# Optimization experiments

Measured on AMD Instinct MI355X. Metric: run time of the kernel, lower is better.

## Reference

```python
import jax, jax.numpy as jnp
import numpy as np

B, S, D, H = 2, 2048, 1024, 16
HD = D // H
SCALE = float(np.sqrt(HD))


def setup_inputs() -> dict:
    key = jax.random.key(0)
    k_x, k_wqkv, k_bqkv, k_wo, k_bo = jax.random.split(key, 5)
    std = 1.0 / np.sqrt(D)
    x = jax.random.normal(k_x, (B, S, D), dtype=jnp.float32)
    mask = jnp.tril(jnp.ones((S, S), dtype=jnp.int32))[None, None]  # (1,1,S,S) causal
    W_qkv = jax.random.normal(k_wqkv, (D, 3 * D), dtype=jnp.float32) * std
    b_qkv = jax.random.normal(k_bqkv, (3 * D,), dtype=jnp.float32) * std
    W_o = jax.random.normal(k_wo, (D, D), dtype=jnp.float32) * std
    b_o = jax.random.normal(k_bo, (D,), dtype=jnp.float32) * std
    return {"x": x, "W_qkv": W_qkv, "b_qkv": b_qkv, "W_o": W_o, "b_o": b_o, "mask": mask}


def reference(x, W_qkv, b_qkv, W_o, b_o, mask):
    # fused QKV projection: (B,S,3D) -> (3,B,H,S,HD)
    qkv = x @ W_qkv + b_qkv
    qkv = qkv.reshape(B, S, 3, H, HD).transpose(2, 0, 3, 1, 4)
    Q, K, V = qkv[0], qkv[1], qkv[2]
    # scaled dot-product attention with explicit mask
    scores = jnp.einsum('bhqd,bhkd->bhqk', Q, K) / SCALE
    scores = jnp.where(mask == 0, -jnp.inf, scores)
    attn = jax.nn.softmax(scores, axis=-1)  # dropout p=0.0 -> identity
    context = jnp.einsum('bhqk,bhkd->bhqd', attn, V)
    context = context.transpose(0, 2, 1, 3).reshape(B, S, D)
    return context @ W_o + b_o
```

## Files before the change

### kernel.cpp

```cpp
#include <hip/hip_runtime.h>
#include <hip/hip_bf16.h>
#include <stdint.h>

#define DEV __device__ __forceinline__

typedef __bf16 bf16x8 __attribute__((ext_vector_type(8)));
typedef float f32x4 __attribute__((ext_vector_type(4)));
typedef float f32x16 __attribute__((ext_vector_type(16)));
typedef unsigned short ushort8 __attribute__((ext_vector_type(8)));

DEV uint16_t f2bf(float f) {
  uint32_t u = __float_as_uint(f);
  u += 0x7fffu + ((u >> 16) & 1u);
  return (uint16_t)(u >> 16);
}

DEV float exp2r(float x) {
  float r;
  asm("v_exp_f32 %0, %1" : "=v"(r) : "v"(x));
  return r;
}

DEV void gload_lds16(const void* g, void* l) {
  __builtin_amdgcn_global_load_lds(
      (const __attribute__((address_space(1))) void*)g,
      (__attribute__((address_space(3))) void*)l, 16, 0, 0);
}

DEV void swap32u(uint32_t& a, uint32_t& b) {
#if defined(__has_builtin) && __has_builtin(__builtin_amdgcn_permlane32_swap)
  auto r = __builtin_amdgcn_permlane32_swap(a, b, false, false);
  a = (uint32_t)r[0];
  b = (uint32_t)r[1];
#else
  uint32_t as = __shfl_xor(a, 32), bs = __shfl_xor(b, 32);
  uint32_t na = (threadIdx.x & 32) ? bs : a;
  uint32_t nb = (threadIdx.x & 32) ? b : as;
  a = na; b = nb;
#endif
}

__global__ __launch_bounds__(256) void k_prep(const float* __restrict__ W0,
                                              uint16_t* __restrict__ WT0,
                                              const float* __restrict__ W1,
                                              uint16_t* __restrict__ WT1,
                                              const float* __restrict__ X,
                                              uint16_t* __restrict__ Xb) {
  const int z = blockIdx.z;
  const int tid = threadIdx.x;
  if (z == 2) {
    const int nt4 = 1048576, stride = 48 * 16 * 256;
    int base = (blockIdx.y * 48 + blockIdx.x) * 256 + tid;
    for (int i = base; i < nt4; i += stride) {
      float4 v = *reinterpret_cast<const float4*>(X + (size_t)i * 4);
      ushort4 o = { f2bf(v.x), f2bf(v.y), f2bf(v.z), f2bf(v.w) };
      *reinterpret_cast<ushort4*>(Xb + (size_t)i * 4) = o;
    }
    return;
  }
  if (z == 1 && blockIdx.x >= 16) return;
  const float* W = z ? W1 : W0;
  uint16_t* WT = z ? WT1 : WT0;
  const int K = 1024, N = z ? 1024 : 3072;
  __shared__ float t[64][65];
  int n0 = blockIdx.x * 64, k0 = blockIdx.y * 64;
  int r = tid >> 4, c4 = (tid & 15) * 4;
#pragma unroll
  for (int p = 0; p < 4; ++p) {
    int kr = p * 16 + r;
    float4 v = *reinterpret_cast<const float4*>(W + (size_t)(k0 + kr) * N + n0 + c4);
    t[kr][c4] = v.x; t[kr][c4 + 1] = v.y; t[kr][c4 + 2] = v.z; t[kr][c4 + 3] = v.w;
  }
  __syncthreads();
#pragma unroll
  for (int p = 0; p < 4; ++p) {
    int nr = p * 16 + r;
    ushort4 o = { f2bf(t[c4][nr]), f2bf(t[c4 + 1][nr]), f2bf(t[c4 + 2][nr]), f2bf(t[c4 + 3][nr]) };
    *reinterpret_cast<ushort4*>(WT + (size_t)(n0 + nr) * K + k0 + c4) = o;
  }
}

__global__ __launch_bounds__(256, 2) void k_gemm0(const uint16_t* __restrict__ A,
                                                  const uint16_t* __restrict__ Bw,
                                                  const float* __restrict__ bias,
                                                  uint16_t* __restrict__ o0,
                                                  uint16_t* __restrict__ o1,
                                                  uint16_t* __restrict__ o2) {
  constexpr int K = 1024;
  __shared__ __attribute__((aligned(16))) char SMEM[65536];
  const int tid = threadIdx.x;
  const int lane = tid & 63, wid = tid >> 6;
  const int g = lane >> 4, c = lane & 15;
  const int nb = gridDim.x * gridDim.y;
  const int bid = blockIdx.y * gridDim.x + blockIdx.x;
  const int cpx = nb >> 3;
  const int swz = (bid & 7) * cpx + (bid >> 3);
  const int bx = swz % gridDim.x, by = swz / gridDim.x;
  const int row0 = by * 128, col0 = bx * 128;
  const int wrow = (wid >> 1) * 64, wcol = (wid & 1) * 64;
  f32x4 acc[4][4] = {};
  const uint16_t* Ag = A + (size_t)row0 * K;
  const uint16_t* Bg = Bw + (size_t)col0 * K;

  const int srow = tid >> 3;
  const int ssw = ((tid & 7) ^ (srow & 7)) * 8;
  auto stageAB = [&](int t, int buf) {
    const int k0 = t * 64;
    char* ab = SMEM + buf * 16384;
    char* bb = SMEM + 32768 + buf * 16384;
#pragma unroll
    for (int i = 0; i < 4; ++i) {
      int row = i * 32 + srow;
      gload_lds16(Ag + (size_t)row * K + k0 + ssw, ab + i * 4096 + tid * 16);
      gload_lds16(Bg + (size_t)row * K + k0 + ssw, bb + i * 4096 + tid * 16);
    }
  };

  stageAB(0, 0);
  asm volatile("s_waitcnt vmcnt(0)" ::: "memory");
  __builtin_amdgcn_s_barrier();
  asm volatile("" ::: "memory");

  for (int t = 0; t < 16; ++t) {
    if (t + 1 < 16) stageAB(t + 1, (t + 1) & 1);
    const uint16_t* Ac = (const uint16_t*)(SMEM + (t & 1) * 16384);
    const uint16_t* Bc = (const uint16_t*)(SMEM + 32768 + (t & 1) * 16384);
    __builtin_amdgcn_s_setprio(1);
#pragma unroll
    for (int kk = 0; kk < 2; ++kk) {
      bf16x8 af[4], bf[4];
#pragma unroll
      for (int m = 0; m < 4; ++m)
        af[m] = *reinterpret_cast<const bf16x8*>(
            &Ac[(wrow + m * 16 + c) * 64 + (((kk * 4 + g) ^ (c & 7)) << 3)]);
#pragma unroll
      for (int n = 0; n < 4; ++n)
        bf[n] = *reinterpret_cast<const bf16x8*>(
            &Bc[(wcol + n * 16 + c) * 64 + (((kk * 4 + g) ^ (c & 7)) << 3)]);
#pragma unroll
      for (int m = 0; m < 4; ++m)
#pragma unroll
        for (int n = 0; n < 4; ++n)
          acc[m][n] = __builtin_amdgcn_mfma_f32_16x16x32_bf16(af[m], bf[n], acc[m][n], 0, 0, 0);
    }
    __builtin_amdgcn_s_setprio(0);
    asm volatile("s_waitcnt vmcnt(0)" ::: "memory");
    __builtin_amdgcn_s_barrier();
    asm volatile("" ::: "memory");
  }

  if (col0 >= 2048) {
    uint16_t* TB = (uint16_t*)SMEM;
#pragma unroll
    for (int n = 0; n < 4; ++n) {
      int col_l = wcol + n * 16 + c;
      float bs = bias[col0 + col_l];
#pragma unroll
      for (int m = 0; m < 4; ++m)
#pragma unroll
        for (int r = 0; r < 4; ++r) {
          int row_l = wrow + m * 16 + g * 4 + r;
          TB[col_l * 136 + row_l] = f2bf(acc[m][n][r] + bs);
        }
    }
    __syncthreads();
    const int col_l = tid >> 1, half = tid & 1;
    const int d = (col0 - 2048) + col_l;
    const int h = d >> 6, hd = d & 63;
    const int b = row0 >> 11, s0 = row0 & 2047;
    uint16_t* dst = o2 + ((size_t)(b * 16 + h) * 64 + hd) * 2048 + s0 + half * 64;
    const uint16_t* src = &TB[col_l * 136 + half * 64];
#pragma unroll
    for (int k = 0; k < 8; ++k) {
      ushort8 v = *reinterpret_cast<const ushort8*>(src + k * 8);
      *reinterpret_cast<ushort8*>(dst + k * 8) = v;
    }
  } else {
#pragma unroll
    for (int m = 0; m < 4; ++m) {
#pragma unroll
      for (int n = 0; n < 4; ++n) {
        int col = col0 + wcol + n * 16 + c;
        float bs = bias[col];
#pragma unroll
        for (int r = 0; r < 4; ++r) {
          int row = row0 + wrow + m * 16 + g * 4 + r;
          float v = acc[m][n][r] + bs;
          int which = col >> 10, d = col & 1023, h = d >> 6, hd = d & 63;
          int b = row >> 11, s = row & 2047;
          int bh = b * 16 + h;
          if (which == 0)      o0[((size_t)bh * 2048 + s) * 64 + hd] = f2bf(v * 0.1803368801111244f);
          else                 o1[((size_t)bh * 2048 + s) * 64 + hd] = f2bf(v);
        }
      }
    }
  }
}

__global__ __launch_bounds__(256, 2) void k_gemm1(const uint16_t* __restrict__ A,
                                                  const uint16_t* __restrict__ Bw,
                                                  const float* __restrict__ bias,
                                                  float* __restrict__ of) {
  constexpr int K = 1024;
  __shared__ __attribute__((aligned(16))) char SMEM[49152];
  const int tid = threadIdx.x;
  const int lane = tid & 63, wid = tid >> 6;
  const int g = lane >> 4, c = lane & 15;
  const int nb = gridDim.x * gridDim.y;
  const int bid = blockIdx.y * gridDim.x + blockIdx.x;
  const int cpx = nb >> 3;
  const int swz = (bid & 7) * cpx + (bid >> 3);
  const int bx = swz % gridDim.x, by = swz / gridDim.x;
  const int row0 = by * 128, col0 = bx * 64;
  f32x4 acc[2][4] = {};
  const uint16_t* Ag = A + (size_t)row0 * K;
  const uint16_t* Bg = Bw + (size_t)col0 * K;

  const int srow = tid >> 3;
  const int ssw = ((tid & 7) ^ (srow & 7)) * 8;
  auto stageAB = [&](int t, int buf) {
    const int k0 = t * 64;
    char* ab = SMEM + buf * 16384;
    char* bb = SMEM + 32768 + buf * 8192;
#pragma unroll
    for (int i = 0; i < 4; ++i)
      gload_lds16(Ag + (size_t)(i * 32 + srow) * K + k0 + ssw, ab + i * 4096 + tid * 16);
#pragma unroll
    for (int i = 0; i < 2; ++i)
      gload_lds16(Bg + (size_t)(i * 32 + srow) * K + k0 + ssw, bb + i * 4096 + tid * 16);
  };

  stageAB(0, 0);
  asm volatile("s_waitcnt vmcnt(0)" ::: "memory");
  __builtin_amdgcn_s_barrier();
  asm volatile("" ::: "memory");

  for (int t = 0; t < 16; ++t) {
    if (t + 1 < 16) stageAB(t + 1, (t + 1) & 1);
    const uint16_t* Ac = (const uint16_t*)(SMEM + (t & 1) * 16384);
    const uint16_t* Bc = (const uint16_t*)(SMEM + 32768 + (t & 1) * 8192);
    __builtin_amdgcn_s_setprio(1);
#pragma unroll
    for (int kk = 0; kk < 2; ++kk) {
      bf16x8 af[2], bf[4];
#pragma unroll
      for (int m = 0; m < 2; ++m)
        af[m] = *reinterpret_cast<const bf16x8*>(
            &Ac[(wid * 32 + m * 16 + c) * 64 + (((kk * 4 + g) ^ (c & 7)) << 3)]);
#pragma unroll
      for (int n = 0; n < 4; ++n)
        bf[n] = *reinterpret_cast<const bf16x8*>(
            &Bc[(n * 16 + c) * 64 + (((kk * 4 + g) ^ (c & 7)) << 3)]);
#pragma unroll
      for (int m = 0; m < 2; ++m)
#pragma unroll
        for (int n = 0; n < 4; ++n)
          acc[m][n] = __builtin_amdgcn_mfma_f32_16x16x32_bf16(af[m], bf[n], acc[m][n], 0, 0, 0);
    }
    __builtin_amdgcn_s_setprio(0);
    asm volatile("s_waitcnt vmcnt(0)" ::: "memory");
    __builtin_amdgcn_s_barrier();
    asm volatile("" ::: "memory");
  }

#pragma unroll
  for (int m = 0; m < 2; ++m) {
#pragma unroll
    for (int n = 0; n < 4; ++n) {
      int col = col0 + n * 16 + c;
      float bs = bias[col];
#pragma unroll
      for (int r = 0; r < 4; ++r) {
        int row = row0 + wid * 32 + m * 16 + g * 4 + r;
        of[(size_t)row * 1024 + col] = acc[m][n][r] + bs;
      }
    }
  }
}

__global__ __launch_bounds__(512, 4) void k_attn(const uint16_t* __restrict__ Qb,
                                                 const uint16_t* __restrict__ Kb,
                                                 const uint16_t* __restrict__ Vb,
                                                 uint16_t* __restrict__ ctx) {
  __shared__ __attribute__((aligned(16))) char SMEM[65536];
  uint16_t* Ksb = (uint16_t*)SMEM;
  uint16_t* Vsb = (uint16_t*)(SMEM + 32768);
  const int bid = blockIdx.x;
  const int xcd = bid & 7;
  const int idx = bid >> 3;
  const int bh = 4 * xcd + (idx & 3);
  const int jj = idx >> 2;
  const int qt = (idx < 32) ? (15 - jj) : (jj - 8);
  const int tid = threadIdx.x, lane = tid & 63, wid = tid >> 6;
  const int qw = wid & 3, kw = wid >> 2;
  const int h2 = lane >> 5, c = lane & 31;
  const int q0 = qt * 128;
  const int qi = q0 + qw * 32 + c;
  const int nt = qt + 1;
  const uint16_t* Qh = Qb + (size_t)bh * 2048 * 64;
  const uint16_t* Kh = Kb + (size_t)bh * 2048 * 64;
  const uint16_t* Vh = Vb + (size_t)bh * 64 * 2048;

  bf16x8 qf[4];
#pragma unroll
  for (int kk = 0; kk < 4; ++kk)
    qf[kk] = *reinterpret_cast<const bf16x8*>(&Qh[(size_t)qi * 64 + kk * 16 + h2 * 8]);

  union OU { uint32_t u[4]; bf16x8 v; } onesu;
  onesu.u[0] = 0x3f803f80u; onesu.u[1] = 0x3f803f80u;
  onesu.u[2] = 0x3f803f80u; onesu.u[3] = 0x3f803f80u;

  f32x16 oT0 = {}, oT1 = {}, lac = {};

  const int srow = tid >> 3;
  const int ssw = ((tid & 7) ^ (srow & 7)) * 8;
  const int vr = tid >> 4;
  const int vsw = ((tid & 15) ^ (vr & 15)) * 8;
  auto stage = [&](int T, int buf) {
    const int j0 = T * 128;
    char* kb = (char*)(Ksb + buf * 8192);
    char* vb = (char*)(Vsb + buf * 8192);
#pragma unroll
    for (int i = 0; i < 2; ++i)
      gload_lds16(Kh + (size_t)(j0 + i * 64 + srow) * 64 + ssw, kb + i * 8192 + tid * 16);
#pragma unroll
    for (int i = 0; i < 2; ++i)
      gload_lds16(Vh + (size_t)(i * 32 + vr) * 2048 + j0 + vsw, vb + i * 8192 + tid * 16);
  };

  union U4 { uint32_t u[4]; bf16x8 v; };

  stage(0, 0);
  asm volatile("s_waitcnt vmcnt(0)" ::: "memory");
  __builtin_amdgcn_s_barrier();
  asm volatile("" ::: "memory");

  for (int T = 0; T < nt; ++T) {
    const int j0 = T * 128;
    if (T + 1 < nt) stage(T + 1, (T + 1) & 1);
    const uint16_t* Kc = Ksb + (T & 1) * 8192;
    const uint16_t* Vc = Vsb + (T & 1) * 8192;
    f32x16 s0 = {}, s1 = {};
    __builtin_amdgcn_s_setprio(1);
#pragma unroll
    for (int kk = 0; kk < 4; ++kk) {
      const int off = ((kk * 2 + h2) ^ (c & 7)) << 3;
      bf16x8 k0 = *reinterpret_cast<const bf16x8*>(&Kc[(kw * 64 + c) * 64 + off]);
      bf16x8 k1 = *reinterpret_cast<const bf16x8*>(&Kc[(kw * 64 + 32 + c) * 64 + off]);
      s0 = __builtin_amdgcn_mfma_f32_32x32x16_bf16(k0, qf[kk], s0, 0, 0, 0);
      s1 = __builtin_amdgcn_mfma_f32_32x32x16_bf16(k1, qf[kk], s1, 0, 0, 0);
    }
    __builtin_amdgcn_s_setprio(0);
    if (T == qt) {
#pragma unroll
      for (int r = 0; r < 16; ++r) {
        int key0 = j0 + kw * 64 + (r & 3) + 8 * (r >> 2) + 4 * h2;
        if (key0 > qi) s0[r] = -INFINITY;
        if (key0 + 32 > qi) s1[r] = -INFINITY;
      }
    }
    uint32_t W[16];
#pragma unroll
    for (int w = 0; w < 8; ++w) {
      float a0 = exp2r(s0[2 * w]), a1 = exp2r(s0[2 * w + 1]);
      float b0 = exp2r(s1[2 * w]), b1 = exp2r(s1[2 * w + 1]);
      asm("v_cvt_pk_bf16_f32 %0, %1, %2" : "=v"(W[w])     : "v"(a0), "v"(a1));
      asm("v_cvt_pk_bf16_f32 %0, %1, %2" : "=v"(W[8 + w]) : "v"(b0), "v"(b1));
    }
#pragma unroll
    for (int cc = 0; cc < 2; ++cc) {
      uint32_t* Wc = &W[cc * 8];
      U4 p0, p1;
      uint32_t a0 = Wc[0], b0 = Wc[2];  swap32u(a0, b0);
      uint32_t a1 = Wc[1], b1 = Wc[3];  swap32u(a1, b1);
      p0.u[0] = a0; p0.u[1] = a1; p0.u[2] = b0; p0.u[3] = b1;
      uint32_t a2 = Wc[4], b2 = Wc[6];  swap32u(a2, b2);
      uint32_t a3 = Wc[5], b3 = Wc[7];  swap32u(a3, b3);
      p1.u[0] = a2; p1.u[1] = a3; p1.u[2] = b2; p1.u[3] = b3;
      const int cb = (kw * 2 + cc) * 4 + h2;
      const int vsl0 = (cb ^ (c & 15)) << 3;
      const int vsl1 = (((cb + 2) & 15) ^ (c & 15)) << 3;
      __builtin_amdgcn_s_setprio(1);
      {
        bf16x8 v0 = *reinterpret_cast<const bf16x8*>(&Vc[c * 128 + vsl0]);
        bf16x8 v1 = *reinterpret_cast<const bf16x8*>(&Vc[c * 128 + vsl1]);
        oT0 = __builtin_amdgcn_mfma_f32_32x32x16_bf16(v0, p0.v, oT0, 0, 0, 0);
        oT0 = __builtin_amdgcn_mfma_f32_32x32x16_bf16(v1, p1.v, oT0, 0, 0, 0);
      }
      {
        bf16x8 v0 = *reinterpret_cast<const bf16x8*>(&Vc[(32 + c) * 128 + vsl0]);
        bf16x8 v1 = *reinterpret_cast<const bf16x8*>(&Vc[(32 + c) * 128 + vsl1]);
        oT1 = __builtin_amdgcn_mfma_f32_32x32x16_bf16(v0, p0.v, oT1, 0, 0, 0);
        oT1 = __builtin_amdgcn_mfma_f32_32x32x16_bf16(v1, p1.v, oT1, 0, 0, 0);
      }
      lac = __builtin_amdgcn_mfma_f32_32x32x16_bf16(onesu.v, p0.v, lac, 0, 0, 0);
      lac = __builtin_amdgcn_mfma_f32_32x32x16_bf16(onesu.v, p1.v, lac, 0, 0, 0);
      __builtin_amdgcn_s_setprio(0);
    }
    asm volatile("s_waitcnt vmcnt(0)" ::: "memory");
    __builtin_amdgcn_s_barrier();
    asm volatile("" ::: "memory");
  }

  float* LB = (float*)SMEM;
  float* OB = LB + 256;
  const int sl = qw * 64 + lane;
  if (kw == 1) {
    LB[sl] = lac[0];
    float* ob = OB + sl * 33;
#pragma unroll
    for (int r = 0; r < 16; ++r) { ob[r] = oT0[r]; ob[16 + r] = oT1[r]; }
  }
  __syncthreads();
  if (kw == 0) {
    const float* ob = OB + sl * 33;
    float inv = 1.0f / (lac[0] + LB[sl]);
    const int b = bh >> 4, h = bh & 15;
    int token = b * 2048 + qi;
    uint16_t* outp = ctx + (size_t)token * 1024 + h * 64;
#pragma unroll
    for (int hb = 0; hb < 2; ++hb) {
      const f32x16& o = hb ? oT1 : oT0;
#pragma unroll
      for (int q4 = 0; q4 < 4; ++q4) {
        ushort4 w;
        w.x = f2bf((o[q4 * 4 + 0] + ob[hb * 16 + q4 * 4 + 0]) * inv);
        w.y = f2bf((o[q4 * 4 + 1] + ob[hb * 16 + q4 * 4 + 1]) * inv);
        w.z = f2bf((o[q4 * 4 + 2] + ob[hb * 16 + q4 * 4 + 2]) * inv);
        w.w = f2bf((o[q4 * 4 + 3] + ob[hb * 16 + q4 * 4 + 3]) * inv);
        *reinterpret_cast<ushort4*>(outp + hb * 32 + 8 * q4 + 4 * h2) = w;
      }
    }
  }
}

extern "C" void kernel_launch(void* const* d_in, const int* in_sizes, int n_in,
                              void* d_out, int out_size, void* d_ws, size_t ws_size,
                              hipStream_t stream) {
  (void)in_sizes; (void)n_in; (void)out_size; (void)ws_size;
  const float* x     = (const float*)d_in[0];
  const float* W_qkv = (const float*)d_in[1];
  const float* b_qkv = (const float*)d_in[2];
  const float* W_o   = (const float*)d_in[3];
  const float* b_o   = (const float*)d_in[4];
  uint16_t* ws    = (uint16_t*)d_ws;
  uint16_t* woT   = ws;
  uint16_t* xb    = woT + 1024 * 1024;
  uint16_t* wqkvT = xb + 4096 * 1024;
  uint16_t* Qb    = wqkvT + 3072 * 1024;
  uint16_t* Kb    = Qb + 32 * 2048 * 64;
  uint16_t* Vb    = Kb + 32 * 2048 * 64;
  uint16_t* ctx   = Vb + 32 * 2048 * 64;

  k_prep<<<dim3(48, 16, 3), 256, 0, stream>>>(W_qkv, wqkvT, W_o, woT, x, xb);
  k_gemm0<<<dim3(24, 32), 256, 0, stream>>>(xb, wqkvT, b_qkv, Qb, Kb, Vb);
  k_attn<<<512, 512, 0, stream>>>(Qb, Kb, Vb, ctx);
  k_gemm1<<<dim3(16, 32), 256, 0, stream>>>(ctx, woT, b_o, (float*)d_out);
}
```

Baseline: 85.81 us.

## Fuse fp32-to-bf16 conversion of x into the QKV GEMM A-tile loads

The separate x-to-bf16 pass in the prep kernel is removed. The QKV GEMM now loads fp32 rows of x into registers, converts them with packed bf16 conversion instructions, and writes them to LDS. B still uses direct global-to-LDS loads. This saves one write and one read of a 4M-element bf16 buffer and some prep-kernel work, but the GEMM now reads twice the A bytes per tile (24 column blocks each re-read fp32 x) and adds register and LDS-write pressure inside the pipelined loop.

Result: slower. 96.39 us (+12.3%).

```diff
diff --git a/kernel.cpp b/kernel.cpp
--- a/kernel.cpp
+++ b/kernel.cpp
@@ -43,21 +43,9 @@
 __global__ __launch_bounds__(256) void k_prep(const float* __restrict__ W0,
                                               uint16_t* __restrict__ WT0,
                                               const float* __restrict__ W1,
-                                              uint16_t* __restrict__ WT1,
-                                              const float* __restrict__ X,
-                                              uint16_t* __restrict__ Xb) {
+                                              uint16_t* __restrict__ WT1) {
   const int z = blockIdx.z;
   const int tid = threadIdx.x;
-  if (z == 2) {
-    const int nt4 = 1048576, stride = 48 * 16 * 256;
-    int base = (blockIdx.y * 48 + blockIdx.x) * 256 + tid;
-    for (int i = base; i < nt4; i += stride) {
-      float4 v = *reinterpret_cast<const float4*>(X + (size_t)i * 4);
-      ushort4 o = { f2bf(v.x), f2bf(v.y), f2bf(v.z), f2bf(v.w) };
-      *reinterpret_cast<ushort4*>(Xb + (size_t)i * 4) = o;
-    }
-    return;
-  }
   if (z == 1 && blockIdx.x >= 16) return;
   const float* W = z ? W1 : W0;
   uint16_t* WT = z ? WT1 : WT0;
@@ -80,7 +68,7 @@
   }
 }
 
-__global__ __launch_bounds__(256, 2) void k_gemm0(const uint16_t* __restrict__ A,
+__global__ __launch_bounds__(256, 2) void k_gemm0(const float* __restrict__ Af,
                                                   const uint16_t* __restrict__ Bw,
                                                   const float* __restrict__ bias,
                                                   uint16_t* __restrict__ o0,
@@ -99,30 +87,53 @@
   const int row0 = by * 128, col0 = bx * 128;
   const int wrow = (wid >> 1) * 64, wcol = (wid & 1) * 64;
   f32x4 acc[4][4] = {};
-  const uint16_t* Ag = A + (size_t)row0 * K;
+  const float* Ag = Af + (size_t)row0 * K;
   const uint16_t* Bg = Bw + (size_t)col0 * K;
 
   const int srow = tid >> 3;
   const int ssw = ((tid & 7) ^ (srow & 7)) * 8;
-  auto stageAB = [&](int t, int buf) {
+  float4 ar[4][2];
+
+  auto stageB = [&](int t, int buf) {
     const int k0 = t * 64;
+    char* bb = SMEM + 32768 + buf * 16384;
+#pragma unroll
+    for (int i = 0; i < 4; ++i)
+      gload_lds16(Bg + (size_t)(i * 32 + srow) * K + k0 + ssw, bb + i * 4096 + tid * 16);
+  };
+  auto loadA = [&](int t) {
+    const int k0 = t * 64;
+#pragma unroll
+    for (int i = 0; i < 4; ++i) {
+      const float* src = Ag + (size_t)(i * 32 + srow) * K + k0 + ssw;
+      ar[i][0] = *reinterpret_cast<const float4*>(src);
+      ar[i][1] = *reinterpret_cast<const float4*>(src + 4);
+    }
+  };
+  auto writeA = [&](int buf) {
     char* ab = SMEM + buf * 16384;
-    char* bb = SMEM + 32768 + buf * 16384;
 #pragma unroll
     for (int i = 0; i < 4; ++i) {
-      int row = i * 32 + srow;
-      gload_lds16(Ag + (size_t)row * K + k0 + ssw, ab + i * 4096 + tid * 16);
-      gload_lds16(Bg + (size_t)row * K + k0 + ssw, bb + i * 4096 + tid * 16);
+      uint32_t w0, w1, w2, w3;
+      asm("v_cvt_pk_bf16_f32 %0, %1, %2" : "=v"(w0) : "v"(ar[i][0].x), "v"(ar[i][0].y));
+      asm("v_cvt_pk_bf16_f32 %0, %1, %2" : "=v"(w1) : "v"(ar[i][0].z), "v"(ar[i][0].w));
+      asm("v_cvt_pk_bf16_f32 %0, %1, %2" : "=v"(w2) : "v"(ar[i][1].x), "v"(ar[i][1].y));
+      asm("v_cvt_pk_bf16_f32 %0, %1, %2" : "=v"(w3) : "v"(ar[i][1].z), "v"(ar[i][1].w));
+      uint4 o = { w0, w1, w2, w3 };
+      *reinterpret_cast<uint4*>(ab + i * 4096 + tid * 16) = o;
     }
   };
 
-  stageAB(0, 0);
+  stageB(0, 0);
+  loadA(0);
   asm volatile("s_waitcnt vmcnt(0)" ::: "memory");
+  writeA(0);
+  asm volatile("s_waitcnt lgkmcnt(0)" ::: "memory");
   __builtin_amdgcn_s_barrier();
   asm volatile("" ::: "memory");
 
   for (int t = 0; t < 16; ++t) {
-    if (t + 1 < 16) stageAB(t + 1, (t + 1) & 1);
+    if (t + 1 < 16) { stageB(t + 1, (t + 1) & 1); loadA(t + 1); }
     const uint16_t* Ac = (const uint16_t*)(SMEM + (t & 1) * 16384);
     const uint16_t* Bc = (const uint16_t*)(SMEM + 32768 + (t & 1) * 16384);
     __builtin_amdgcn_s_setprio(1);
@@ -145,6 +156,8 @@
     }
     __builtin_amdgcn_s_setprio(0);
     asm volatile("s_waitcnt vmcnt(0)" ::: "memory");
+    if (t + 1 < 16) writeA((t + 1) & 1);
+    asm volatile("s_waitcnt lgkmcnt(0)" ::: "memory");
     __builtin_amdgcn_s_barrier();
     asm volatile("" ::: "memory");
   }
@@ -445,15 +458,14 @@
   const float* b_o   = (const float*)d_in[4];
   uint16_t* ws    = (uint16_t*)d_ws;
   uint16_t* woT   = ws;
-  uint16_t* xb    = woT + 1024 * 1024;
-  uint16_t* wqkvT = xb + 4096 * 1024;
+  uint16_t* wqkvT = woT + 1024 * 1024;
   uint16_t* Qb    = wqkvT + 3072 * 1024;
   uint16_t* Kb    = Qb + 32 * 2048 * 64;
   uint16_t* Vb    = Kb + 32 * 2048 * 64;
   uint16_t* ctx   = Vb + 32 * 2048 * 64;
 
-  k_prep<<<dim3(48, 16, 3), 256, 0, stream>>>(W_qkv, wqkvT, W_o, woT, x, xb);
-  k_gemm0<<<dim3(24, 32), 256, 0, stream>>>(xb, wqkvT, b_qkv, Qb, Kb, Vb);
+  k_prep<<<dim3(48, 16, 2), 256, 0, stream>>>(W_qkv, wqkvT, W_o, woT);
+  k_gemm0<<<dim3(24, 32), 256, 0, stream>>>(x, wqkvT, b_qkv, Qb, Kb, Vb);
   k_attn<<<512, 512, 0, stream>>>(Qb, Kb, Vb, ctx);
   k_gemm1<<<dim3(16, 32), 256, 0, stream>>>(ctx, woT, b_o, (float*)d_out);
 }
```
